# Kernel optimization log

Hardware: AMD Instinct MI355X
Metric: run time of the kernel (lower is better)

## Reference

```python
import jax, jax.numpy as jnp
import numpy as np

N = 50000      # nodes
E = 800000     # edges (avg degree 16)
IN, H, C = 256, 128, 64
LPA_ITER = 10


def setup_inputs() -> dict:
    key = jax.random.key(0)
    ks = jax.random.split(key, 8)
    x = jax.random.normal(ks[0], (N, IN), dtype=jnp.float32)
    soft_labels = jax.random.uniform(ks[1], (N, C), dtype=jnp.float32)
    edge_index = jax.random.randint(ks[2], (2, E), 0, N, dtype=jnp.int64)
    edge_attr = jax.random.uniform(ks[3], (E,), dtype=jnp.float32)  # abs(edge_weights), positive
    W1 = jax.random.normal(ks[4], (IN, H), dtype=jnp.float32) * (1.0 / np.sqrt(IN))
    b1 = jnp.zeros((H,), dtype=jnp.float32)
    W2 = jax.random.normal(ks[5], (H, C), dtype=jnp.float32) * (1.0 / np.sqrt(H))
    b2 = jnp.zeros((C,), dtype=jnp.float32)
    return {"x": x, "soft_labels": soft_labels, "edge_index": edge_index,
            "edge_attr": edge_attr, "W1": W1, "b1": b1, "W2": W2, "b2": b2}


def reference(x, soft_labels, edge_index, edge_attr, W1, b1, W2, b2):
    row, col = edge_index[0], edge_index[1]
    # Row-normalize sparse adjacency: deg[i] = sum of edge values in row i,
    # value <- value / deg[row]  (deg^-1 with inf -> 0)
    deg = jax.ops.segment_sum(edge_attr, row, num_segments=N)
    deg_inv = jnp.where(deg > 0, 1.0 / deg, 0.0)
    val = edge_attr * deg_inv[row]  # [E]

    def spmm(m):
        # out[i] = sum_{(i,j) in E} A[i,j] * m[j]
        return jax.ops.segment_sum(val[:, None] * m[col], row, num_segments=N)

    # GCNConv(normalize=False): spmm(A, x @ W) + b ; dropout is identity in eval mode
    h = jax.nn.relu(spmm(x @ W1) + b1)
    out = spmm(h @ W2) + b2

    # Label propagation: lpa_iter sparse-dense spmm steps
    labels = soft_labels
    for _ in range(LPA_ITER):
        labels = spmm(labels)
    return out, labels
```

## Files before the change

### kernel.cpp

```cpp
#include <hip/hip_runtime.h>

#define NN 50000
#define EE 800000
#define FIN 256
#define FH 128
#define FC 64
#define LPA_ITERS 10
#define NBLK 196
#define G1X 782
#define SPB 3125
#define SP128B 6250
#define EBLK 3125

typedef __attribute__((ext_vector_type(8))) short short8v;
typedef __attribute__((ext_vector_type(4))) float f32x4;

__device__ __forceinline__ int edge_at(const int* __restrict__ ei, int is32, int which, int e) {
    int idx = which * EE + e;
    return is32 ? ei[idx] : ei[2 * idx];
}

__global__ void detect_k(const unsigned int* __restrict__ w, int* __restrict__ flag) {
    int any = 0;
    for (int i = 1 + 2 * (int)threadIdx.x; i < 2048; i += 2 * (int)blockDim.x)
        if (w[i] != 0u) any = 1;
    if (any) atomicOr(flag, 1);
}

__device__ __forceinline__ unsigned short bf16_rne(float f) {
    unsigned u = __float_as_uint(f);
    return (unsigned short)((u + 0x7FFFu + ((u >> 16) & 1u)) >> 16);
}
__device__ __forceinline__ unsigned packbf2(float a, float b) {
    return (unsigned)bf16_rne(a) | ((unsigned)bf16_rne(b) << 16);
}

__device__ __forceinline__ void accum_body(int pb, const int* __restrict__ ei,
                                           const int* __restrict__ flag,
                                           int* __restrict__ cnt,
                                           int* __restrict__ slot) {
    int e = pb * 256 + (int)threadIdx.x;
    if (e >= EE) return;
    int is32 = *flag;
    int r = edge_at(ei, is32, 0, e);
    slot[e] = atomicAdd(&cnt[r], 1);
}

__global__ __launch_bounds__(256) void scan1_k(const int* __restrict__ cnt,
                                               int* __restrict__ start,
                                               int* __restrict__ bsum,
                                               int* __restrict__ blockhist) {
    __shared__ int wtot[4];
    __shared__ int hist[64];
    int t = threadIdx.x, blk = blockIdx.x;
    int i = blk * 256 + t;
    if (t < 64) hist[t] = 0;
    __syncthreads();
    int c = (i < NN) ? cnt[i] : 0;
    if (i < NN) atomicAdd(&hist[c < 63 ? c : 63], 1);
    int lane = t & 63, w = t >> 6;
    int s = c;
    for (int d = 1; d < 64; d <<= 1) {
        int u = __shfl_up(s, d, 64);
        if (lane >= d) s += u;
    }
    if (lane == 63) wtot[w] = s;
    __syncthreads();
    int woff = 0;
    for (int j = 0; j < 4; ++j)
        if (j < w) woff += wtot[j];
    int excl = s - c + woff;
    if (i < NN) start[i] = excl;
    if (t == 255) bsum[blk] = excl + c;
    if (t < 64) blockhist[t * NBLK + blk] = hist[t];
}

__global__ void scan2_k(int* __restrict__ bsum, int* __restrict__ blockhist) {
    __shared__ int wtot[4];
    __shared__ int btot[64];
    int t = threadIdx.x;
    int lane = t & 63, w = t >> 6;
    int v = (t < NBLK) ? bsum[t] : 0;
    int s = v;
    for (int d = 1; d < 64; d <<= 1) {
        int u = __shfl_up(s, d, 64);
        if (lane >= d) s += u;
    }
    if (lane == 63) wtot[w] = s;
    __syncthreads();
    int woff = 0;
    for (int j = 0; j < 4; ++j)
        if (j < w) woff += wtot[j];
    if (t < NBLK) bsum[t] = s - v + woff;
    if (t < 64) {
        int run = 0;
        for (int j = 0; j < NBLK; ++j) {
            int idx = t * NBLK + j;
            int tmp = blockhist[idx];
            blockhist[idx] = run;
            run += tmp;
        }
        btot[t] = run;
    }
    __syncthreads();
    if (t < 64) {
        int bv = btot[t];
        int bs = bv;
        for (int d = 1; d < 64; d <<= 1) {
            int u = __shfl_up(bs, d, 64);
            if (lane >= d) bs += u;
        }
        int base = bs - bv;
        for (int j = 0; j < NBLK; ++j) blockhist[t * NBLK + j] += base;
    }
}

__global__ __launch_bounds__(256) void finish_k(const int* __restrict__ cnt,
                                                int* __restrict__ start,
                                                const int* __restrict__ bsum,
                                                const int* __restrict__ blockhist,
                                                int* __restrict__ perm) {
    __shared__ int hist[64];
    int t = threadIdx.x, blk = blockIdx.x;
    int i = blk * 256 + t;
    if (t < 64) hist[t] = 0;
    __syncthreads();
    if (i < NN) {
        start[i] += bsum[blk];
        int c = cnt[i];
        int b = c < 63 ? c : 63;
        int rank = atomicAdd(&hist[b], 1);
        perm[blockhist[b * NBLK + blk] + rank] = i;
    }
}

__global__ __launch_bounds__(256) void scatter_k(const int* __restrict__ ei,
                                                 const int* __restrict__ flag,
                                                 const float* __restrict__ ea,
                                                 const int* __restrict__ start,
                                                 const int* __restrict__ slot,
                                                 uint2* __restrict__ csr) {
    int e = blockIdx.x * 256 + threadIdx.x;
    if (e >= EE) return;
    int is32 = *flag;
    int r = edge_at(ei, is32, 0, e);
    int c = edge_at(ei, is32, 1, e);
    csr[start[r] + slot[e]] = make_uint2((unsigned)c, __float_as_uint(ea[e]));
}

__global__ __launch_bounds__(256) void rowscale_k(const int* __restrict__ start,
                                                  const int* __restrict__ cnt,
                                                  const uint2* __restrict__ csr,
                                                  float* __restrict__ deginv) {
    int t = threadIdx.x;
    int r = blockIdx.x * 16 + (t >> 4);
    if (r >= NN) return;
    int fl = t & 15;
    int s = start[r], n = cnt[r];
    float sum = 0.f;
    for (int k = fl; k < n; k += 16) sum += __uint_as_float(csr[s + k].y);
    for (int d = 1; d < 16; d <<= 1) sum += __shfl_xor(sum, d, 16);
    if (fl == 0) deginv[r] = sum > 0.f ? 1.f / sum : 0.f;
}

__global__ __launch_bounds__(256) void wcvt_k(const float* __restrict__ W,
                                              short* __restrict__ hi,
                                              short* __restrict__ lo,
                                              int K, int N) {
    int i = blockIdx.x * 256 + threadIdx.x;
    if (i >= K * N) return;
    int k = i / N, n = i - k * N;
    float f = W[i];
    unsigned short h = bf16_rne(f);
    float hf = __uint_as_float((unsigned)h << 16);
    unsigned short l = bf16_rne(f - hf);
    hi[n * K + k] = (short)h;
    lo[n * K + k] = (short)l;
}

__global__ __launch_bounds__(256) void cast_k(const float* __restrict__ in,
                                              uint2* __restrict__ outb, int n4) {
    int i = blockIdx.x * 256 + threadIdx.x;
    if (i >= n4) return;
    float4 f = ((const float4*)in)[i];
    outb[i] = make_uint2(packbf2(f.x, f.y), packbf2(f.z, f.w));
}


template <int KDIM, int NCOLT, int NF, int ABF, int CBF>
__device__ __forceinline__ void mgemm2_body(int bx, int cb,
                                            const void* __restrict__ Ap,
                                            const short* __restrict__ Bhi0,
                                            const short* __restrict__ Blo0,
                                            void* __restrict__ Cp, int M) {
    static_assert((size_t)NF * 16 * 72 * 2 * 2 < 49152, "LDS must stay well under 64KB");
    __shared__ short bh[NF * 16][72];
    __shared__ short bl[NF * 16][72];
    const int NSTG = KDIM / 64;
    const int NCH = NF / 2;
    int t = threadIdx.x;
    const short* Bhi = Bhi0 + (size_t)cb * (NF * 16) * KDIM;
    const short* Blo = Blo0 + (size_t)cb * (NF * 16) * KDIM;
    int wid = t >> 6, l = t & 63, l15 = l & 15, lq = l >> 4;
    int row = bx * 64 + wid * 16 + l15;
    bool rv = row < M;
    f32x4 acc[NF];
#pragma unroll
    for (int j = 0; j < NF; ++j) acc[j] = (f32x4){0.f, 0.f, 0.f, 0.f};

    short8v rh[NCH], rl[NCH];
    float4 af[2][4];
    short8v ab_[2][2];
#pragma unroll
    for (int b = 0; b < 2; ++b) {
        if (ABF) {
            ab_[b][0] = (short8v){0, 0, 0, 0, 0, 0, 0, 0};
            ab_[b][1] = (short8v){0, 0, 0, 0, 0, 0, 0, 0};
        } else {
#pragma unroll
            for (int q = 0; q < 4; ++q) af[b][q] = make_float4(0.f, 0.f, 0.f, 0.f);
        }
    }

    auto loadB = [&](int k0) {
#pragma unroll
        for (int j = 0; j < NCH; ++j) {
            int c = t + j * 256;
            int col = c >> 3;
            int kk = (c & 7) * 8;
            rh[j] = *(const short8v*)&Bhi[(size_t)col * KDIM + k0 + kk];
            rl[j] = *(const short8v*)&Blo[(size_t)col * KDIM + k0 + kk];
        }
    };
    auto loadA = [&](int k0, int buf) {
        if (!rv) return;
        if (ABF) {
            const short* A = (const short*)Ap;
            ab_[buf][0] = *(const short8v*)&A[(size_t)row * KDIM + k0 + 8 * lq];
            ab_[buf][1] = *(const short8v*)&A[(size_t)row * KDIM + k0 + 32 + 8 * lq];
        } else {
            const float* A = (const float*)Ap;
            const float4* p0 = (const float4*)&A[(size_t)row * KDIM + k0 + 8 * lq];
            af[buf][0] = p0[0];
            af[buf][1] = p0[1];
            const float4* p1 = (const float4*)&A[(size_t)row * KDIM + k0 + 32 + 8 * lq];
            af[buf][2] = p1[0];
            af[buf][3] = p1[1];
        }
    };

    loadB(0);
    loadA(0, 0);
#pragma unroll
    for (int sg = 0; sg < NSTG; ++sg) {
        __syncthreads();
#pragma unroll
        for (int j = 0; j < NCH; ++j) {
            int c = t + j * 256;
            int col = c >> 3;
            int kk = (c & 7) * 8;
            *(short8v*)&bh[col][kk] = rh[j];
            *(short8v*)&bl[col][kk] = rl[j];
        }
        __syncthreads();
        if (sg + 1 < NSTG) {
            loadB((sg + 1) * 64);
            loadA((sg + 1) * 64, (sg + 1) & 1);
        }
        int cbuf = sg & 1;
#pragma unroll
        for (int ks = 0; ks < 2; ++ks) {
            short8v ahi, alo;
            if (ABF) {
                ahi = ab_[cbuf][ks];
            } else {
                float av[8];
                float4 xa = af[cbuf][ks * 2], xb = af[cbuf][ks * 2 + 1];
                av[0] = xa.x; av[1] = xa.y; av[2] = xa.z; av[3] = xa.w;
                av[4] = xb.x; av[5] = xb.y; av[6] = xb.z; av[7] = xb.w;
#pragma unroll
                for (int e = 0; e < 8; ++e) {
                    unsigned short h = bf16_rne(av[e]);
                    float hf = __uint_as_float((unsigned)h << 16);
                    ahi[e] = (short)h;
                    alo[e] = (short)bf16_rne(av[e] - hf);
                }
            }
#pragma unroll
            for (int j = 0; j < NF; ++j) {
                int col = j * 16 + l15;
                short8v fh = *(const short8v*)&bh[col][ks * 32 + 8 * lq];
                short8v fo = *(const short8v*)&bl[col][ks * 32 + 8 * lq];
                acc[j] = __builtin_amdgcn_mfma_f32_16x16x32_bf16(ahi, fh, acc[j], 0, 0, 0);
                acc[j] = __builtin_amdgcn_mfma_f32_16x16x32_bf16(ahi, fo, acc[j], 0, 0, 0);
                if (!ABF)
                    acc[j] = __builtin_amdgcn_mfma_f32_16x16x32_bf16(alo, fh, acc[j], 0, 0, 0);
            }
        }
    }
    int rbase = bx * 64 + wid * 16 + 4 * lq;
#pragma unroll
    for (int j = 0; j < NF; ++j) {
        int col = cb * (NF * 16) + j * 16 + l15;
#pragma unroll
        for (int e = 0; e < 4; ++e) {
            int r = rbase + e;
            if (r < M) {
                if (CBF)
                    ((unsigned short*)Cp)[(size_t)r * NCOLT + col] = bf16_rne(acc[j][e]);
                else
                    ((float*)Cp)[(size_t)r * NCOLT + col] = acc[j][e];
            }
        }
    }
}

__device__ __forceinline__ void spmm64f_body(int pb, const int* __restrict__ perm,
                                             const int* __restrict__ start,
                                             const int* __restrict__ cnt,
                                             const float* __restrict__ deginv,
                                             const uint2* __restrict__ csr,
                                             const float* __restrict__ m,
                                             float* __restrict__ out,
                                             const float* __restrict__ bias) {
    int t = threadIdx.x;
    int p = pb * 16 + (t >> 4);
    if (p >= NN) return;
    int r = perm[p];
    int fl = t & 15;
    const float4* m4 = (const float4*)m;
    float4 acc = make_float4(0.f, 0.f, 0.f, 0.f);
    int s = start[r], n = cnt[r];
    int k = 0;
    for (; k + 8 <= n; k += 8) {
        uint2 ev[8];
        float4 gv[8];
#pragma unroll
        for (int u = 0; u < 8; ++u) ev[u] = csr[s + k + u];
#pragma unroll
        for (int u = 0; u < 8; ++u) gv[u] = m4[(size_t)ev[u].x * 16 + fl];
#pragma unroll
        for (int u = 0; u < 8; ++u) {
            float v = __uint_as_float(ev[u].y);
            acc.x = fmaf(v, gv[u].x, acc.x); acc.y = fmaf(v, gv[u].y, acc.y);
            acc.z = fmaf(v, gv[u].z, acc.z); acc.w = fmaf(v, gv[u].w, acc.w);
        }
    }
    for (; k < n; ++k) {
        uint2 e = csr[s + k];
        float v = __uint_as_float(e.y);
        float4 g = m4[(size_t)e.x * 16 + fl];
        acc.x = fmaf(v, g.x, acc.x); acc.y = fmaf(v, g.y, acc.y);
        acc.z = fmaf(v, g.z, acc.z); acc.w = fmaf(v, g.w, acc.w);
    }
    float dv = deginv[r];
    acc.x *= dv; acc.y *= dv; acc.z *= dv; acc.w *= dv;
    float4 b = ((const float4*)bias)[fl];
    acc.x += b.x; acc.y += b.y; acc.z += b.z; acc.w += b.w;
    ((float4*)out)[(size_t)r * 16 + fl] = acc;
}

__device__ __forceinline__ void spmm128b_body(int pb, const int* __restrict__ perm,
                                              const int* __restrict__ start,
                                              const int* __restrict__ cnt,
                                              const float* __restrict__ deginv,
                                              const uint2* __restrict__ csr,
                                              const uint2* __restrict__ mb,
                                              uint2* __restrict__ outb,
                                              const float* __restrict__ bias) {
    int t = threadIdx.x;
    int p = pb * 8 + (t >> 5);
    if (p >= NN) return;
    int r = perm[p];
    int fl = t & 31;
    float4 acc = make_float4(0.f, 0.f, 0.f, 0.f);
    int s = start[r], n = cnt[r];
    int k = 0;
    for (; k + 8 <= n; k += 8) {
        uint2 ev[8];
        uint2 gv[8];
#pragma unroll
        for (int u = 0; u < 8; ++u) ev[u] = csr[s + k + u];
#pragma unroll
        for (int u = 0; u < 8; ++u) gv[u] = mb[(size_t)ev[u].x * 32 + fl];
#pragma unroll
        for (int u = 0; u < 8; ++u) {
            float v = __uint_as_float(ev[u].y);
            acc.x = fmaf(v, __uint_as_float(gv[u].x << 16), acc.x);
            acc.y = fmaf(v, __uint_as_float(gv[u].x & 0xFFFF0000u), acc.y);
            acc.z = fmaf(v, __uint_as_float(gv[u].y << 16), acc.z);
            acc.w = fmaf(v, __uint_as_float(gv[u].y & 0xFFFF0000u), acc.w);
        }
    }
    for (; k < n; ++k) {
        uint2 e = csr[s + k];
        float v = __uint_as_float(e.y);
        uint2 g = mb[(size_t)e.x * 32 + fl];
        acc.x = fmaf(v, __uint_as_float(g.x << 16), acc.x);
        acc.y = fmaf(v, __uint_as_float(g.x & 0xFFFF0000u), acc.y);
        acc.z = fmaf(v, __uint_as_float(g.y << 16), acc.z);
        acc.w = fmaf(v, __uint_as_float(g.y & 0xFFFF0000u), acc.w);
    }
    float dv = deginv[r];
    float4 b = ((const float4*)bias)[fl];
    acc.x = fmaxf(fmaf(acc.x, dv, b.x), 0.f);
    acc.y = fmaxf(fmaf(acc.y, dv, b.y), 0.f);
    acc.z = fmaxf(fmaf(acc.z, dv, b.z), 0.f);
    acc.w = fmaxf(fmaf(acc.w, dv, b.w), 0.f);
    outb[(size_t)r * 32 + fl] = make_uint2(packbf2(acc.x, acc.y), packbf2(acc.z, acc.w));
}

__device__ __forceinline__ void spmm64b_body(int pb, const int* __restrict__ perm,
                                             const int* __restrict__ start,
                                             const int* __restrict__ cnt,
                                             const float* __restrict__ deginv,
                                             const uint2* __restrict__ csr,
                                             const uint2* __restrict__ mb,
                                             void* __restrict__ outp, int f32out) {
    int t = threadIdx.x;
    int p = pb * 16 + (t >> 4);
    if (p >= NN) return;
    int r = perm[p];
    int fl = t & 15;
    float4 acc = make_float4(0.f, 0.f, 0.f, 0.f);
    int s = start[r], n = cnt[r];
    int k = 0;
    for (; k + 8 <= n; k += 8) {
        uint2 ev[8];
        uint2 gv[8];
#pragma unroll
        for (int u = 0; u < 8; ++u) ev[u] = csr[s + k + u];
#pragma unroll
        for (int u = 0; u < 8; ++u) gv[u] = mb[(size_t)ev[u].x * 16 + fl];
#pragma unroll
        for (int u = 0; u < 8; ++u) {
            float v = __uint_as_float(ev[u].y);
            acc.x = fmaf(v, __uint_as_float(gv[u].x << 16), acc.x);
            acc.y = fmaf(v, __uint_as_float(gv[u].x & 0xFFFF0000u), acc.y);
            acc.z = fmaf(v, __uint_as_float(gv[u].y << 16), acc.z);
            acc.w = fmaf(v, __uint_as_float(gv[u].y & 0xFFFF0000u), acc.w);
        }
    }
    for (; k < n; ++k) {
        uint2 e = csr[s + k];
        float v = __uint_as_float(e.y);
        uint2 g = mb[(size_t)e.x * 16 + fl];
        acc.x = fmaf(v, __uint_as_float(g.x << 16), acc.x);
        acc.y = fmaf(v, __uint_as_float(g.x & 0xFFFF0000u), acc.y);
        acc.z = fmaf(v, __uint_as_float(g.y << 16), acc.z);
        acc.w = fmaf(v, __uint_as_float(g.y & 0xFFFF0000u), acc.w);
    }
    float dv = deginv[r];
    acc.x *= dv; acc.y *= dv; acc.z *= dv; acc.w *= dv;
    if (f32out) {
        ((float4*)outp)[(size_t)r * 16 + fl] = acc;
    } else {
        ((uint2*)outp)[(size_t)r * 16 + fl] =
            make_uint2(packbf2(acc.x, acc.y), packbf2(acc.z, acc.w));
    }
}


__global__ __launch_bounds__(256) void fa_k(const float* __restrict__ x,
                                            const short* __restrict__ w1h,
                                            const short* __restrict__ w1l,
                                            unsigned short* __restrict__ t1,
                                            const int* __restrict__ ei,
                                            const int* __restrict__ flag,
                                            int* __restrict__ cnt,
                                            int* __restrict__ slot) {
    int b = blockIdx.x;
    if (b < 2 * G1X)
        mgemm2_body<FIN, FH, 4, 0, 1>(b % G1X, b / G1X, x, w1h, w1l, t1, NN);
    else
        accum_body(b - 2 * G1X, ei, flag, cnt, slot);
}

__global__ __launch_bounds__(256) void f2_k(const int* __restrict__ perm,
                                            const int* __restrict__ start,
                                            const int* __restrict__ cnt,
                                            const float* __restrict__ dinv,
                                            const uint2* __restrict__ csr,
                                            const uint2* __restrict__ t1,
                                            uint2* __restrict__ h,
                                            const float* __restrict__ b1,
                                            const uint2* __restrict__ sbf,
                                            uint2* __restrict__ lA) {
    int b = blockIdx.x;
    if (b < SP128B)
        spmm128b_body(b, perm, start, cnt, dinv, csr, t1, h, b1);
    else
        spmm64b_body(b - SP128B, perm, start, cnt, dinv, csr, sbf, lA, 0);
}

__global__ __launch_bounds__(256) void f3_k(const unsigned short* __restrict__ h,
                                            const short* __restrict__ w2h,
                                            const short* __restrict__ w2l,
                                            float* __restrict__ t2,
                                            const int* __restrict__ perm,
                                            const int* __restrict__ start,
                                            const int* __restrict__ cnt,
                                            const float* __restrict__ dinv,
                                            const uint2* __restrict__ csr,
                                            const uint2* __restrict__ lA,
                                            uint2* __restrict__ lB) {
    int b = blockIdx.x;
    if (b < G1X)
        mgemm2_body<FH, FC, 4, 1, 0>(b, 0, h, w2h, w2l, t2, NN);
    else
        spmm64b_body(b - G1X, perm, start, cnt, dinv, csr, lA, lB, 0);
}

__global__ __launch_bounds__(256) void f4_k(const int* __restrict__ perm,
                                            const int* __restrict__ start,
                                            const int* __restrict__ cnt,
                                            const float* __restrict__ dinv,
                                            const uint2* __restrict__ csr,
                                            const float* __restrict__ t2,
                                            float* __restrict__ out,
                                            const float* __restrict__ b2,
                                            const uint2* __restrict__ lB,
                                            uint2* __restrict__ lA) {
    int b = blockIdx.x;
    if (b < SPB)
        spmm64f_body(b, perm, start, cnt, dinv, csr, t2, out, b2);
    else
        spmm64b_body(b - SPB, perm, start, cnt, dinv, csr, lB, lA, 0);
}

__global__ __launch_bounds__(256) void spmm64b_k(const int* __restrict__ perm,
                                                 const int* __restrict__ start,
                                                 const int* __restrict__ cnt,
                                                 const float* __restrict__ deginv,
                                                 const uint2* __restrict__ csr,
                                                 const uint2* __restrict__ mb,
                                                 void* __restrict__ outp,
                                                 int f32out) {
    spmm64b_body(blockIdx.x, perm, start, cnt, deginv, csr, mb, outp, f32out);
}

extern "C" void kernel_launch(void* const* d_in, const int* in_sizes, int n_in,
                              void* d_out, int out_size, void* d_ws, size_t ws_size,
                              hipStream_t stream) {
    const float* x    = (const float*)d_in[0];
    const float* soft = (const float*)d_in[1];
    const int*   ei   = (const int*)d_in[2];
    const float* ea   = (const float*)d_in[3];
    const float* W1   = (const float*)d_in[4];
    const float* b1   = (const float*)d_in[5];
    const float* W2   = (const float*)d_in[6];
    const float* b2   = (const float*)d_in[7];
    float* out  = (float*)d_out;
    float* labB = out + (size_t)NN * FC;

    char* ws = (char*)d_ws;
    size_t off = 0;
    auto alloc = [&](size_t b) { size_t o = off; off += (b + 255) & ~(size_t)255; return o; };
    size_t o_misc  = alloc(256);
    size_t o_cnt   = alloc((size_t)NN * 4);
    size_t zero_end = off;
    size_t o_start = alloc((size_t)NN * 4);
    size_t o_perm  = alloc((size_t)NN * 4);
    size_t o_dinv  = alloc((size_t)NN * 4);
    size_t o_bsum  = alloc((size_t)NBLK * 4);
    size_t o_bhist = alloc((size_t)64 * NBLK * 4);
    size_t o_slot  = alloc((size_t)EE * 4);
    size_t o_csr   = alloc((size_t)EE * 8);
    size_t o_w1h   = alloc((size_t)FIN * FH * 2);
    size_t o_w1l   = alloc((size_t)FIN * FH * 2);
    size_t o_w2h   = alloc((size_t)FH * FC * 2);
    size_t o_w2l   = alloc((size_t)FH * FC * 2);
    size_t o_t1    = alloc((size_t)NN * FH * 2);
    size_t o_h     = alloc((size_t)NN * FH * 2);
    size_t o_t2    = alloc((size_t)NN * FC * 4);
    size_t o_sbf   = alloc((size_t)NN * FC * 2);
    size_t o_lA    = alloc((size_t)NN * FC * 2);
    size_t o_lB    = alloc((size_t)NN * FC * 2);
    if (off > ws_size) return;

    int*   misc  = (int*)(ws + o_misc);
    int*   cnt   = (int*)(ws + o_cnt);
    int*   start = (int*)(ws + o_start);
    int*   perm  = (int*)(ws + o_perm);
    float* dinv  = (float*)(ws + o_dinv);
    int*   bsum  = (int*)(ws + o_bsum);
    int*   bhist = (int*)(ws + o_bhist);
    int*   slot  = (int*)(ws + o_slot);
    uint2* csr   = (uint2*)(ws + o_csr);
    short* w1h   = (short*)(ws + o_w1h);
    short* w1l   = (short*)(ws + o_w1l);
    short* w2h   = (short*)(ws + o_w2h);
    short* w2l   = (short*)(ws + o_w2l);
    unsigned short* t1 = (unsigned short*)(ws + o_t1);
    uint2* h     = (uint2*)(ws + o_h);
    float* t2    = (float*)(ws + o_t2);
    uint2* sbf   = (uint2*)(ws + o_sbf);
    uint2* lA    = (uint2*)(ws + o_lA);
    uint2* lB    = (uint2*)(ws + o_lB);

    hipMemsetAsync(d_ws, 0, zero_end, stream);
    detect_k<<<1, 256, 0, stream>>>((const unsigned int*)ei, &misc[0]);
    wcvt_k<<<(FIN * FH + 255) / 256, 256, 0, stream>>>(W1, w1h, w1l, FIN, FH);
    wcvt_k<<<(FH * FC + 255) / 256, 256, 0, stream>>>(W2, w2h, w2l, FH, FC);
    cast_k<<<(NN * FC / 4 + 255) / 256, 256, 0, stream>>>(soft, sbf, NN * FC / 4);

    fa_k<<<2 * G1X + EBLK, 256, 0, stream>>>(x, w1h, w1l, t1, ei, misc, cnt, slot);

    scan1_k<<<NBLK, 256, 0, stream>>>(cnt, start, bsum, bhist);
    scan2_k<<<1, 256, 0, stream>>>(bsum, bhist);
    finish_k<<<NBLK, 256, 0, stream>>>(cnt, start, bsum, bhist, perm);
    scatter_k<<<(EE + 255) / 256, 256, 0, stream>>>(ei, misc, ea, start, slot, csr);
    rowscale_k<<<(NN + 15) / 16, 256, 0, stream>>>(start, cnt, csr, dinv);

    f2_k<<<SP128B + SPB, 256, 0, stream>>>(perm, start, cnt, dinv, csr,
                                           (const uint2*)t1, h, b1, sbf, lA);
    f3_k<<<G1X + SPB, 256, 0, stream>>>((const unsigned short*)h, w2h, w2l, t2,
                                        perm, start, cnt, dinv, csr, lA, lB);
    f4_k<<<SPB + SPB, 256, 0, stream>>>(perm, start, cnt, dinv, csr, t2, out, b2,
                                        lB, lA);

    const uint2* src = lA;
    uint2* dst = lB;
    for (int it = 3; it < LPA_ITERS; ++it) {
        int last = (it == LPA_ITERS - 1);
        spmm64b_k<<<SPB, 256, 0, stream>>>(perm, start, cnt, dinv, csr, src,
                                           last ? (void*)labB : (void*)dst, last);
        src = dst;
        dst = (dst == lA) ? lB : lA;
    }
}
```

Baseline: 350.9 us.

## Spread GEMM1 blocks across CSR-build kernels and merge prep kernels into one

```diff
diff --git a/kernel.cpp b/kernel.cpp
--- a/kernel.cpp
+++ b/kernel.cpp
@@ -12,19 +12,17 @@
 #define SP128B 6250
 #define EBLK 3125
 
+#define G1_S1 782
+#define G1_S2 882
+#define G1_S3 1382
+#define G1_TOT 1564
+
 typedef __attribute__((ext_vector_type(8))) short short8v;
 typedef __attribute__((ext_vector_type(4))) float f32x4;
 
 __device__ __forceinline__ int edge_at(const int* __restrict__ ei, int is32, int which, int e) {
     int idx = which * EE + e;
     return is32 ? ei[idx] : ei[2 * idx];
-}
-
-__global__ void detect_k(const unsigned int* __restrict__ w, int* __restrict__ flag) {
-    int any = 0;
-    for (int i = 1 + 2 * (int)threadIdx.x; i < 2048; i += 2 * (int)blockDim.x)
-        if (w[i] != 0u) any = 1;
-    if (any) atomicOr(flag, 1);
 }
 
 __device__ __forceinline__ unsigned short bf16_rne(float f) {
@@ -115,13 +113,13 @@
     }
 }
 
-__global__ __launch_bounds__(256) void finish_k(const int* __restrict__ cnt,
-                                                int* __restrict__ start,
-                                                const int* __restrict__ bsum,
-                                                const int* __restrict__ blockhist,
-                                                int* __restrict__ perm) {
+__device__ __forceinline__ void finish_body(int blk, const int* __restrict__ cnt,
+                                            int* __restrict__ start,
+                                            const int* __restrict__ bsum,
+                                            const int* __restrict__ blockhist,
+                                            int* __restrict__ perm) {
     __shared__ int hist[64];
-    int t = threadIdx.x, blk = blockIdx.x;
+    int t = threadIdx.x;
     int i = blk * 256 + t;
     if (t < 64) hist[t] = 0;
     __syncthreads();
@@ -134,13 +132,13 @@
     }
 }
 
-__global__ __launch_bounds__(256) void scatter_k(const int* __restrict__ ei,
-                                                 const int* __restrict__ flag,
-                                                 const float* __restrict__ ea,
-                                                 const int* __restrict__ start,
-                                                 const int* __restrict__ slot,
-                                                 uint2* __restrict__ csr) {
-    int e = blockIdx.x * 256 + threadIdx.x;
+__device__ __forceinline__ void scatter_body(int pb, const int* __restrict__ ei,
+                                             const int* __restrict__ flag,
+                                             const float* __restrict__ ea,
+                                             const int* __restrict__ start,
+                                             const int* __restrict__ slot,
+                                             uint2* __restrict__ csr) {
+    int e = pb * 256 + (int)threadIdx.x;
     if (e >= EE) return;
     int is32 = *flag;
     int r = edge_at(ei, is32, 0, e);
@@ -148,12 +146,12 @@
     csr[start[r] + slot[e]] = make_uint2((unsigned)c, __float_as_uint(ea[e]));
 }
 
-__global__ __launch_bounds__(256) void rowscale_k(const int* __restrict__ start,
-                                                  const int* __restrict__ cnt,
-                                                  const uint2* __restrict__ csr,
-                                                  float* __restrict__ deginv) {
+__device__ __forceinline__ void rowscale_body(int pb, const int* __restrict__ start,
+                                              const int* __restrict__ cnt,
+                                              const uint2* __restrict__ csr,
+                                              float* __restrict__ deginv) {
     int t = threadIdx.x;
-    int r = blockIdx.x * 16 + (t >> 4);
+    int r = pb * 16 + (t >> 4);
     if (r >= NN) return;
     int fl = t & 15;
     int s = start[r], n = cnt[r];
@@ -163,29 +161,42 @@
     if (fl == 0) deginv[r] = sum > 0.f ? 1.f / sum : 0.f;
 }
 
-__global__ __launch_bounds__(256) void wcvt_k(const float* __restrict__ W,
-                                              short* __restrict__ hi,
-                                              short* __restrict__ lo,
-                                              int K, int N) {
-    int i = blockIdx.x * 256 + threadIdx.x;
-    if (i >= K * N) return;
-    int k = i / N, n = i - k * N;
-    float f = W[i];
-    unsigned short h = bf16_rne(f);
-    float hf = __uint_as_float((unsigned)h << 16);
-    unsigned short l = bf16_rne(f - hf);
-    hi[n * K + k] = (short)h;
-    lo[n * K + k] = (short)l;
-}
-
-__global__ __launch_bounds__(256) void cast_k(const float* __restrict__ in,
-                                              uint2* __restrict__ outb, int n4) {
-    int i = blockIdx.x * 256 + threadIdx.x;
-    if (i >= n4) return;
-    float4 f = ((const float4*)in)[i];
-    outb[i] = make_uint2(packbf2(f.x, f.y), packbf2(f.z, f.w));
-}
-
+__global__ __launch_bounds__(256) void prep_k(const float* __restrict__ W1,
+                                              const float* __restrict__ W2,
+                                              const float* __restrict__ soft,
+                                              const unsigned int* __restrict__ eiw,
+                                              int* __restrict__ flag,
+                                              short* __restrict__ w1h, short* __restrict__ w1l,
+                                              short* __restrict__ w2h, short* __restrict__ w2l,
+                                              uint2* __restrict__ sbf) {
+    int b = blockIdx.x, t = threadIdx.x;
+    if (b < 3125) {
+        int i = b * 256 + t;
+        float4 f = ((const float4*)soft)[i];
+        sbf[i] = make_uint2(packbf2(f.x, f.y), packbf2(f.z, f.w));
+    } else if (b < 3125 + 128) {
+        int i = (b - 3125) * 256 + t;
+        int k = i / FH, n = i - k * FH;
+        float f = W1[i];
+        unsigned short h = bf16_rne(f);
+        float hf = __uint_as_float((unsigned)h << 16);
+        w1h[n * FIN + k] = (short)h;
+        w1l[n * FIN + k] = (short)bf16_rne(f - hf);
+    } else if (b < 3125 + 128 + 32) {
+        int i = (b - 3125 - 128) * 256 + t;
+        int k = i / FC, n = i - k * FC;
+        float f = W2[i];
+        unsigned short h = bf16_rne(f);
+        float hf = __uint_as_float((unsigned)h << 16);
+        w2h[n * FH + k] = (short)h;
+        w2l[n * FH + k] = (short)bf16_rne(f - hf);
+    } else {
+        int any = 0;
+        for (int i = 1 + 2 * t; i < 2048; i += 512)
+            if (eiw[i] != 0u) any = 1;
+        if (any) atomicOr(flag, 1);
+    }
+}
 
 template <int KDIM, int NCOLT, int NF, int ABF, int CBF>
 __device__ __forceinline__ void mgemm2_body(int bx, int cb,
@@ -313,6 +324,13 @@
             }
         }
     }
+}
+
+__device__ __forceinline__ void gemm1_v(int v, const float* __restrict__ x,
+                                        const short* __restrict__ w1h,
+                                        const short* __restrict__ w1l,
+                                        unsigned short* __restrict__ t1) {
+    mgemm2_body<FIN, FH, 4, 0, 1>(v % G1X, v / G1X, x, w1h, w1l, t1, NN);
 }
 
 __device__ __forceinline__ void spmm64f_body(int pb, const int* __restrict__ perm,
@@ -461,7 +479,7 @@
 }
 
 
-__global__ __launch_bounds__(256) void fa_k(const float* __restrict__ x,
+__global__ __launch_bounds__(256) void p1_k(const float* __restrict__ x,
                                             const short* __restrict__ w1h,
                                             const short* __restrict__ w1l,
                                             unsigned short* __restrict__ t1,
@@ -470,10 +488,50 @@
                                             int* __restrict__ cnt,
                                             int* __restrict__ slot) {
     int b = blockIdx.x;
-    if (b < 2 * G1X)
-        mgemm2_body<FIN, FH, 4, 0, 1>(b % G1X, b / G1X, x, w1h, w1l, t1, NN);
-    else
-        accum_body(b - 2 * G1X, ei, flag, cnt, slot);
+    if (b < G1_S1) gemm1_v(b, x, w1h, w1l, t1);
+    else accum_body(b - G1_S1, ei, flag, cnt, slot);
+}
+
+__global__ __launch_bounds__(256) void p2_k(const float* __restrict__ x,
+                                            const short* __restrict__ w1h,
+                                            const short* __restrict__ w1l,
+                                            unsigned short* __restrict__ t1,
+                                            const int* __restrict__ cnt,
+                                            int* __restrict__ start,
+                                            const int* __restrict__ bsum,
+                                            const int* __restrict__ bhist,
+                                            int* __restrict__ perm) {
+    int b = blockIdx.x;
+    if (b < G1_S2 - G1_S1) gemm1_v(G1_S1 + b, x, w1h, w1l, t1);
+    else finish_body(b - (G1_S2 - G1_S1), cnt, start, bsum, bhist, perm);
+}
+
+__global__ __launch_bounds__(256) void p3_k(const float* __restrict__ x,
+                                            const short* __restrict__ w1h,
+                                            const short* __restrict__ w1l,
+                                            unsigned short* __restrict__ t1,
+                                            const int* __restrict__ ei,
+                                            const int* __restrict__ flag,
+                                            const float* __restrict__ ea,
+                                            const int* __restrict__ start,
+                                            const int* __restrict__ slot,
+                                            uint2* __restrict__ csr) {
+    int b = blockIdx.x;
+    if (b < G1_S3 - G1_S2) gemm1_v(G1_S2 + b, x, w1h, w1l, t1);
+    else scatter_body(b - (G1_S3 - G1_S2), ei, flag, ea, start, slot, csr);
+}
+
+__global__ __launch_bounds__(256) void p4_k(const float* __restrict__ x,
+                                            const short* __restrict__ w1h,
+                                            const short* __restrict__ w1l,
+                                            unsigned short* __restrict__ t1,
+                                            const int* __restrict__ start,
+                                            const int* __restrict__ cnt,
+                                            const uint2* __restrict__ csr,
+                                            float* __restrict__ dinv) {
+    int b = blockIdx.x;
+    if (b < G1_TOT - G1_S3) gemm1_v(G1_S3 + b, x, w1h, w1l, t1);
+    else rowscale_body(b - (G1_TOT - G1_S3), start, cnt, csr, dinv);
 }
 
 __global__ __launch_bounds__(256) void f2_k(const int* __restrict__ perm,
@@ -599,18 +657,18 @@
     uint2* lB    = (uint2*)(ws + o_lB);
 
     hipMemsetAsync(d_ws, 0, zero_end, stream);
-    detect_k<<<1, 256, 0, stream>>>((const unsigned int*)ei, &misc[0]);
-    wcvt_k<<<(FIN * FH + 255) / 256, 256, 0, stream>>>(W1, w1h, w1l, FIN, FH);
-    wcvt_k<<<(FH * FC + 255) / 256, 256, 0, stream>>>(W2, w2h, w2l, FH, FC);
-    cast_k<<<(NN * FC / 4 + 255) / 256, 256, 0, stream>>>(soft, sbf, NN * FC / 4);
-
-    fa_k<<<2 * G1X + EBLK, 256, 0, stream>>>(x, w1h, w1l, t1, ei, misc, cnt, slot);
-
+    prep_k<<<3125 + 128 + 32 + 1, 256, 0, stream>>>(W1, W2, soft, (const unsigned int*)ei,
+                                                    &misc[0], w1h, w1l, w2h, w2l, sbf);
+
+    p1_k<<<G1_S1 + EBLK, 256, 0, stream>>>(x, w1h, w1l, t1, ei, misc, cnt, slot);
     scan1_k<<<NBLK, 256, 0, stream>>>(cnt, start, bsum, bhist);
     scan2_k<<<1, 256, 0, stream>>>(bsum, bhist);
-    finish_k<<<NBLK, 256, 0, stream>>>(cnt, start, bsum, bhist, perm);
-    scatter_k<<<(EE + 255) / 256, 256, 0, stream>>>(ei, misc, ea, start, slot, csr);
-    rowscale_k<<<(NN + 15) / 16, 256, 0, stream>>>(start, cnt, csr, dinv);
+    p2_k<<<(G1_S2 - G1_S1) + NBLK, 256, 0, stream>>>(x, w1h, w1l, t1, cnt, start, bsum,
+                                                     bhist, perm);
+    p3_k<<<(G1_S3 - G1_S2) + EBLK, 256, 0, stream>>>(x, w1h, w1l, t1, ei, misc, ea,
+                                                     start, slot, csr);
+    p4_k<<<(G1_TOT - G1_S3) + SPB, 256, 0, stream>>>(x, w1h, w1l, t1, start, cnt, csr,
+                                                     dinv);
 
     f2_k<<<SP128B + SPB, 256, 0, stream>>>(perm, start, cnt, dinv, csr,
                                            (const uint2*)t1, h, b1, sbf, lA);
```

New measurement: 351.8 us. Within noise of the previous version (+0.3%).
